# Performance work log

Measured on AMD Instinct MI355X. Metric: run time of the kernel, lower is better.

## Reference

```python
import jax, jax.numpy as jnp
import numpy as np

N_NODES, N_EDGES = 50000, 400000
F_IN, H, L, C = 8, 64, 3, 1
E_IN = 2 * H + 1 + 1  # feats_i, feats_j, edge_attr(1), rel_dist(1)


def setup_inputs() -> dict:
    key = jax.random.key(0)
    ks = jax.random.split(key, 16)
    s = 0.05
    return {
        "x": jax.random.normal(ks[0], (N_NODES, F_IN), jnp.float32),
        "pos": jax.random.normal(ks[1], (N_NODES, 3), jnp.float32),
        "edge_index": jax.random.randint(ks[2], (2, N_EDGES), 0, N_NODES),
        "edge_attr": jax.random.normal(ks[3], (N_EDGES, 1), jnp.float32),
        "embedW": jax.random.normal(ks[4], (F_IN, H), jnp.float32) * s,
        "embedb": jnp.zeros((H,), jnp.float32),
        "eW1": jax.random.normal(ks[5], (L, E_IN, 2 * E_IN), jnp.float32) * s,
        "eb1": jnp.zeros((L, 2 * E_IN), jnp.float32),
        "eW2": jax.random.normal(ks[6], (L, 2 * E_IN, H), jnp.float32) * s,
        "eb2": jnp.zeros((L, H), jnp.float32),
        "cW1": jax.random.normal(ks[7], (L, H, 4 * H), jnp.float32) * s,
        "cb1": jnp.zeros((L, 4 * H), jnp.float32),
        "cW2": jax.random.normal(ks[8], (L, 4 * H, 1), jnp.float32) * s,
        "cb2": jnp.zeros((L, 1), jnp.float32),
        "nW1": jax.random.normal(ks[9], (L, 2 * H, 2 * H), jnp.float32) * s,
        "nb1": jnp.zeros((L, 2 * H), jnp.float32),
        "nW2": jax.random.normal(ks[10], (L, 2 * H, H), jnp.float32) * s,
        "nb2": jnp.zeros((L, H), jnp.float32),
        "linW": jax.random.normal(ks[11], (H, C), jnp.float32) * s,
        "linb": jnp.zeros((C,), jnp.float32),
    }


def reference(x, pos, edge_index, edge_attr, embedW, embedb,
              eW1, eb1, eW2, eb2, cW1, cb1, cW2, cb2,
              nW1, nb1, nW2, nb2, linW, linb):
    silu = jax.nn.silu
    row, col = edge_index[0], edge_index[1]  # target i, source j
    feats = x @ embedW + embedb              # [N, H] initial node embedding
    coors = pos                              # [N, 3]
    for l in range(L):  # fixed small layer loop
        rel = coors[row] - coors[col]                            # [E, 3]
        dist = jnp.sum(rel * rel, axis=-1, keepdims=True)        # [E, 1]
        e_in = jnp.concatenate([feats[row], feats[col], edge_attr, dist], axis=-1)
        # edge_mlp: Linear -> SiLU -> Linear -> SiLU
        m = silu(silu(e_in @ eW1[l] + eb1[l]) @ eW2[l] + eb2[l])  # [E, H]
        # coors_mlp: Linear -> SiLU -> Linear -> scalar weight per edge
        cw = silu(m @ cW1[l] + cb1[l]) @ cW2[l] + cb2[l]          # [E, 1]
        coors = coors + jax.ops.segment_sum(cw * rel, row, num_segments=N_NODES)
        m_i = jax.ops.segment_sum(m, row, num_segments=N_NODES)  # [N, H]
        h = jnp.concatenate([feats, m_i], axis=-1)                # [N, 2H]
        # node_mlp: Linear -> SiLU -> Linear, residual on feats
        feats = feats + (silu(h @ nW1[l] + nb1[l]) @ nW2[l] + nb2[l])
    return feats @ linW + linb  # [N, C]
```

## Files before the change

kernel.cpp:

```cpp
#include <hip/hip_runtime.h>
#include <hip/hip_bf16.h>

#define NN 50000
#define NNP 50048
#define NE 400000
#define FH 64
#define NTILES (NE / 64)
#define CHUNK 782

typedef __attribute__((ext_vector_type(8))) short short8;
typedef __attribute__((ext_vector_type(8))) _Float16 half8;
typedef __attribute__((ext_vector_type(4))) float float4v;

__device__ __forceinline__ float silu_f(float x) {
    return x * __builtin_amdgcn_rcpf(1.0f + __expf(-x));
}
__device__ __forceinline__ short f2h(float f) {
    _Float16 h = (_Float16)f;
    return *(short*)&h;
}
__device__ __forceinline__ float h2f(short s) {
    _Float16 h = *(_Float16*)&s;
    return (float)h;
}

__device__ __forceinline__ void frag_body(const float* __restrict__ src,
                                          short* __restrict__ dst,
                                          int t, int K, int N, int KT, int dup,
                                          int perL, int srcL) {
    int l = t / perL, tt = t - l * perL;
    int j = tt & 7, lane = (tt >> 3) & 63, frag = tt >> 9;
    int nt = frag / KT, kt = frag - nt * KT;
    int k = kt * 32 + ((lane >> 4) << 3) + j;
    int n = nt * 16 + (lane & 15);
    if (k == dup) k = dup - 1;
    float v = (k < K && n < N) ? src[(size_t)l * srcL + k * N + n] : 0.f;
    dst[t] = f2h(v);
}

__global__ void prep_all(const float* __restrict__ eW1, const float* __restrict__ eW2,
                         const float* __restrict__ cW1, const float* __restrict__ nW1,
                         const float* __restrict__ nW2, const float* __restrict__ eb1,
                         short* W1f, short* W2f, short* cW1f, short* nW1f,
                         short* nW2f, float* b1p, int* __restrict__ deg) {
    int t = blockIdx.x * 256 + threadIdx.x;
    if (t < 130560) { frag_body(eW1, W1f, t, 131, 260, 5, 130, 43520, 33800); return; }
    t -= 130560;
    if (t < 55296) { frag_body(eW2, W2f, t, 260, 64, 9, -1, 18432, 16640); return; }
    t -= 55296;
    if (t < 49152) { frag_body(cW1, cW1f, t, 64, 256, 2, -1, 16384, 16384); return; }
    t -= 49152;
    if (t < 49152) { frag_body(nW1, nW1f, t, 128, 128, 4, -1, 16384, 16384); return; }
    t -= 49152;
    if (t < 24576) { frag_body(nW2, nW2f, t, 128, 64, 4, -1, 8192, 8192); return; }
    t -= 24576;
    if (t < 816) { int l = t / 272, c = t - l * 272; b1p[t] = (c < 260) ? eb1[l * 260 + c] : 0.f; return; }
    t -= 816;
    if (t < NN + 1) deg[t] = 0;
}

__global__ void embed_kernel(const float* __restrict__ x, const float* __restrict__ W,
                             const float* __restrict__ b, const float* __restrict__ pos,
                             float* __restrict__ feats, short* __restrict__ featsh,
                             float* __restrict__ cA) {
    int t = blockIdx.x * 256 + threadIdx.x;
    if (t >= NN * FH) return;
    int n = t >> 6, hcol = t & 63;
    float acc = b[hcol];
    #pragma unroll
    for (int k = 0; k < 8; k++) acc += x[n * 8 + k] * W[k * FH + hcol];
    feats[t] = acc;
    featsh[t] = f2h(acc);
    if (hcol < 3) cA[n * 3 + hcol] = pos[n * 3 + hcol];
}

__global__ void hist_kernel(const int* __restrict__ ei, int* __restrict__ deg) {
    int e = blockIdx.x * 256 + threadIdx.x;
    if (e >= NE) return;
    atomicAdd(&deg[ei[e]], 1);
}

__global__ void alloc_kernel(const int* __restrict__ deg, int* __restrict__ off,
                             int* __restrict__ cursor, int* __restrict__ gcount) {
    __shared__ int s[256];
    __shared__ int base;
    int t = threadIdx.x, n = blockIdx.x * 256 + t;
    int d = (n < NN) ? deg[n] : 0;
    s[t] = d;
    __syncthreads();
    for (int st = 1; st < 256; st <<= 1) {
        int v = (t >= st) ? s[t - st] : 0;
        __syncthreads();
        s[t] += v;
        __syncthreads();
    }
    if (t == 255) base = atomicAdd(gcount, s[255]);
    __syncthreads();
    if (n < NN) { int o = base + s[t] - d; off[n] = o; cursor[n] = o; }
}

__global__ void fill_kernel(const int* __restrict__ ei, const float* __restrict__ eattr,
                            int* __restrict__ cursor, int* __restrict__ erow,
                            int* __restrict__ ecol, float* __restrict__ eattrp) {
    int e = blockIdx.x * 256 + threadIdx.x;
    if (e >= NE) return;
    int r = ei[e];
    int p = atomicAdd(&cursor[r], 1);
    erow[p] = r;
    ecol[p] = ei[NE + e];
    eattrp[p] = eattr[e];
}

#define SE_STRIDE 168
#define H1_STRIDE 296
#define M_STRIDE  72

__global__ __launch_bounds__(256, 3) void edge_fused(
    const int* __restrict__ erow, const int* __restrict__ ecol,
    const float* __restrict__ eattrp,
    const short* __restrict__ featsh, const float* __restrict__ coors,
    const short* __restrict__ W1f, const float* __restrict__ b1p,
    const short* __restrict__ W2f, const float* __restrict__ b2,
    const short* __restrict__ cW1f, const float* __restrict__ cb1,
    const float* __restrict__ cW2, const float* __restrict__ cb2,
    short* __restrict__ m_edge, float* __restrict__ cwrel, int do_cw)
{
    __shared__ char smem[48896];
    short* sE   = (short*)smem;
    short* sH1  = (short*)smem;
    short* sM   = (short*)(smem + 37888);
    float* sRel = (float*)(smem + 47104);
    float* cwbuf = (float*)(smem + 47872);

    int b = blockIdx.x;
    int kb = (b & 7) * CHUNK + (b >> 3);
    if (kb >= NTILES) return;
    int k0 = kb * 64;

    int t = threadIdx.x;
    int lane = t & 63, wid = t >> 6, quad = lane >> 4, lc = lane & 15;

    {
        int el = t >> 2, sub = t & 3, k = k0 + el;
        int rI = erow[k], cI = ecol[k];
        const short8* fr = (const short8*)(featsh + (size_t)rI * FH);
        const short8* fc = (const short8*)(featsh + (size_t)cI * FH);
        short* er = sE + el * SE_STRIDE;
        *(short8*)(er + sub * 16) = fr[sub * 2];
        *(short8*)(er + sub * 16 + 8) = fr[sub * 2 + 1];
        *(short8*)(er + 64 + sub * 16) = fc[sub * 2];
        *(short8*)(er + 64 + sub * 16 + 8) = fc[sub * 2 + 1];
        #pragma unroll
        for (int i = 0; i < 10; i++) er[128 + sub * 10 + i] = 0;
        if (sub == 0) {
            float rx = coors[rI * 3 + 0] - coors[cI * 3 + 0];
            float ry = coors[rI * 3 + 1] - coors[cI * 3 + 1];
            float rz = coors[rI * 3 + 2] - coors[cI * 3 + 2];
            float dist = rx * rx + ry * ry + rz * rz;
            short dh = f2h(dist);
            er[128] = f2h(eattrp[k]);
            er[129] = dh;
            er[130] = f2h(dist - h2f(dh));
            sRel[el * 3 + 0] = rx; sRel[el * 3 + 1] = ry; sRel[el * 3 + 2] = rz;
        }
    }
    __syncthreads();

    half8 af[4][5];
    #pragma unroll
    for (int m = 0; m < 4; m++)
        #pragma unroll
        for (int kt = 0; kt < 5; kt++)
            af[m][kt] = *(const half8*)(sE + (m * 16 + lc) * SE_STRIDE + kt * 32 + quad * 8);
    __syncthreads();

    {
        *(long long*)(sH1 + (t >> 2) * H1_STRIDE + 272 + (t & 3) * 4) = 0LL;
        #pragma unroll
        for (int i = 0; i < 4; i++) {
            int nt = wid + i * 4;
            float bias = b1p[nt * 16 + lc];
            float4v acc[4];
            #pragma unroll
            for (int m = 0; m < 4; m++) acc[m] = (float4v){bias, bias, bias, bias};
            #pragma unroll
            for (int kt = 0; kt < 5; kt++) {
                half8 bh = ((const half8*)(W1f + (size_t)(nt * 5 + kt) * 512))[lane];
                #pragma unroll
                for (int m = 0; m < 4; m++)
                    acc[m] = __builtin_amdgcn_mfma_f32_16x16x32_f16(af[m][kt], bh, acc[m], 0, 0, 0);
            }
            #pragma unroll
            for (int m = 0; m < 4; m++)
                #pragma unroll
                for (int r = 0; r < 4; r++)
                    sH1[(m * 16 + quad * 4 + r) * H1_STRIDE + nt * 16 + lc] = f2h(silu_f(acc[m][r]));
        }
        if (wid == 0) {
            const int nt = 16;
            float bias = b1p[nt * 16 + lc];
            float4v acc[4];
            #pragma unroll
            for (int m = 0; m < 4; m++) acc[m] = (float4v){bias, bias, bias, bias};
            #pragma unroll
            for (int kt = 0; kt < 5; kt++) {
                half8 bh = ((const half8*)(W1f + (size_t)(nt * 5 + kt) * 512))[lane];
                #pragma unroll
                for (int m = 0; m < 4; m++)
                    acc[m] = __builtin_amdgcn_mfma_f32_16x16x32_f16(af[m][kt], bh, acc[m], 0, 0, 0);
            }
            #pragma unroll
            for (int m = 0; m < 4; m++)
                #pragma unroll
                for (int r = 0; r < 4; r++)
                    sH1[(m * 16 + quad * 4 + r) * H1_STRIDE + nt * 16 + lc] = f2h(silu_f(acc[m][r]));
        }
    }
    __syncthreads();

    {
        int nt = wid;
        float bias = b2[nt * 16 + lc];
        float4v acc[4];
        #pragma unroll
        for (int m = 0; m < 4; m++) acc[m] = (float4v){bias, bias, bias, bias};
        #pragma unroll
        for (int kt = 0; kt < 9; kt++) {
            half8 bh = ((const half8*)(W2f + (size_t)(nt * 9 + kt) * 512))[lane];
            #pragma unroll
            for (int m = 0; m < 4; m++) {
                half8 a = *(const half8*)(sH1 + (m * 16 + lc) * H1_STRIDE + kt * 32 + quad * 8);
                acc[m] = __builtin_amdgcn_mfma_f32_16x16x32_f16(a, bh, acc[m], 0, 0, 0);
            }
        }
        #pragma unroll
        for (int m = 0; m < 4; m++)
            #pragma unroll
            for (int r = 0; r < 4; r++)
                sM[(m * 16 + quad * 4 + r) * M_STRIDE + nt * 16 + lc] = f2h(silu_f(acc[m][r]));
    }
    __syncthreads();

    {
        int row = t >> 2, c0 = (t & 3) * 16;
        short8 v0 = *(const short8*)(sM + row * M_STRIDE + c0);
        short8 v1 = *(const short8*)(sM + row * M_STRIDE + c0 + 8);
        short* mg = m_edge + (size_t)(k0 + row) * FH + c0;
        *(short8*)(mg) = v0;
        *(short8*)(mg + 8) = v1;
    }
    if (do_cw) {
        half8 ag[4][2];
        #pragma unroll
        for (int m = 0; m < 4; m++)
            #pragma unroll
            for (int kt = 0; kt < 2; kt++)
                ag[m][kt] = *(const half8*)(sM + (m * 16 + lc) * M_STRIDE + kt * 32 + quad * 8);
        float cwpart[4][4];
        #pragma unroll
        for (int m = 0; m < 4; m++)
            #pragma unroll
            for (int r = 0; r < 4; r++) cwpart[m][r] = 0.f;
        #pragma unroll
        for (int i = 0; i < 4; i++) {
            int nt = wid + i * 4;
            float bias = cb1[nt * 16 + lc];
            float4v acc[4];
            #pragma unroll
            for (int m = 0; m < 4; m++) acc[m] = (float4v){bias, bias, bias, bias};
            #pragma unroll
            for (int kt = 0; kt < 2; kt++) {
                half8 bh = ((const half8*)(cW1f + (size_t)(nt * 2 + kt) * 512))[lane];
                #pragma unroll
                for (int m = 0; m < 4; m++)
                    acc[m] = __builtin_amdgcn_mfma_f32_16x16x32_f16(ag[m][kt], bh, acc[m], 0, 0, 0);
            }
            float wv = cW2[nt * 16 + lc];
            #pragma unroll
            for (int m = 0; m < 4; m++)
                #pragma unroll
                for (int r = 0; r < 4; r++)
                    cwpart[m][r] += silu_f(acc[m][r]) * wv;
        }
        #pragma unroll
        for (int m = 0; m < 4; m++)
            #pragma unroll
            for (int r = 0; r < 4; r++) {
                float p = cwpart[m][r];
                p += __shfl_xor(p, 1);
                p += __shfl_xor(p, 2);
                p += __shfl_xor(p, 4);
                p += __shfl_xor(p, 8);
                if (lc == 0) cwbuf[wid * 64 + m * 16 + quad * 4 + r] = p;
            }
        __syncthreads();

        if (t < 64) {
            float cw = cb2[0] + cwbuf[t] + cwbuf[64 + t] + cwbuf[128 + t] + cwbuf[192 + t];
            float* o = cwrel + (size_t)(k0 + t) * 3;
            o[0] = cw * sRel[t * 3 + 0];
            o[1] = cw * sRel[t * 3 + 1];
            o[2] = cw * sRel[t * 3 + 2];
        }
    }
}

#define HS 136
__global__ __launch_bounds__(256, 4) void agg_node(
    const int* __restrict__ off, const int* __restrict__ deg,
    const short* __restrict__ m_edge, const float* __restrict__ cwrel,
    const float* __restrict__ coors_in, float* __restrict__ coors_out,
    float* __restrict__ feats, short* __restrict__ featsh,
    const short* __restrict__ W1f, const float* __restrict__ b1,
    const short* __restrict__ W2f, const float* __restrict__ b2,
    const float* __restrict__ linW, const float* __restrict__ linb,
    float* __restrict__ out, int last)
{
    __shared__ short sh[64 * HS];
    __shared__ short sg[64 * HS];
    int t = threadIdx.x, lane = t & 63, wid = t >> 6, quad = lane >> 4, lc = lane & 15;
    int n0 = blockIdx.x * 64;

    {
        int row = t >> 2, sub = t & 3;
        const short8* fp = (const short8*)(featsh + (size_t)(n0 + row) * FH);
        *(short8*)(sh + row * HS + sub * 16) = fp[sub * 2];
        *(short8*)(sh + row * HS + sub * 16 + 8) = fp[sub * 2 + 1];
    }
    for (int nn = 0; nn < 16; nn++) {
        int row = wid * 16 + nn;
        int n = n0 + row;
        float sum = 0.f, cv = 0.f;
        if (n < NN) {
            int s = off[n], e = s + deg[n];
            float s0 = 0.f, s1 = 0.f, s2 = 0.f, s3 = 0.f;
            int k = s;
            for (; k + 3 < e; k += 4) {
                s0 += h2f(m_edge[(size_t)k * FH + lane]);
                s1 += h2f(m_edge[(size_t)(k + 1) * FH + lane]);
                s2 += h2f(m_edge[(size_t)(k + 2) * FH + lane]);
                s3 += h2f(m_edge[(size_t)(k + 3) * FH + lane]);
                if (!last && lane < 3)
                    cv += (cwrel[(size_t)k * 3 + lane] + cwrel[(size_t)(k + 1) * 3 + lane])
                        + (cwrel[(size_t)(k + 2) * 3 + lane] + cwrel[(size_t)(k + 3) * 3 + lane]);
            }
            for (; k < e; k++) {
                s0 += h2f(m_edge[(size_t)k * FH + lane]);
                if (!last && lane < 3) cv += cwrel[(size_t)k * 3 + lane];
            }
            sum = (s0 + s1) + (s2 + s3);
            if (!last && lane < 3) coors_out[n * 3 + lane] = coors_in[n * 3 + lane] + cv;
        }
        sh[row * HS + 64 + lane] = f2h(sum);
    }
    __syncthreads();

    half8 af[4][4];
    #pragma unroll
    for (int m = 0; m < 4; m++)
        #pragma unroll
        for (int kt = 0; kt < 4; kt++)
            af[m][kt] = *(const half8*)(sh + (m * 16 + lc) * HS + kt * 32 + quad * 8);
    #pragma unroll
    for (int i = 0; i < 2; i++) {
        int nt = wid + i * 4;
        float bias = b1[nt * 16 + lc];
        float4v acc[4];
        #pragma unroll
        for (int m = 0; m < 4; m++) acc[m] = (float4v){bias, bias, bias, bias};
        #pragma unroll
        for (int kt = 0; kt < 4; kt++) {
            half8 bh = ((const half8*)(W1f + (size_t)(nt * 4 + kt) * 512))[lane];
            #pragma unroll
            for (int m = 0; m < 4; m++)
                acc[m] = __builtin_amdgcn_mfma_f32_16x16x32_f16(af[m][kt], bh, acc[m], 0, 0, 0);
        }
        #pragma unroll
        for (int m = 0; m < 4; m++)
            #pragma unroll
            for (int r = 0; r < 4; r++)
                sg[(m * 16 + quad * 4 + r) * HS + nt * 16 + lc] = f2h(silu_f(acc[m][r]));
    }
    __syncthreads();

    {
        int nt = wid;
        float bias = b2[nt * 16 + lc];
        float4v acc[4];
        #pragma unroll
        for (int m = 0; m < 4; m++) acc[m] = (float4v){bias, bias, bias, bias};
        #pragma unroll
        for (int kt = 0; kt < 4; kt++) {
            half8 bh = ((const half8*)(W2f + (size_t)(nt * 4 + kt) * 512))[lane];
            #pragma unroll
            for (int m = 0; m < 4; m++) {
                half8 a = *(const half8*)(sg + (m * 16 + lc) * HS + kt * 32 + quad * 8);
                acc[m] = __builtin_amdgcn_mfma_f32_16x16x32_f16(a, bh, acc[m], 0, 0, 0);
            }
        }
        if (!last) {
            #pragma unroll
            for (int m = 0; m < 4; m++)
                #pragma unroll
                for (int r = 0; r < 4; r++) {
                    int row = m * 16 + quad * 4 + r;
                    size_t idx = (size_t)(n0 + row) * FH + nt * 16 + lc;
                    float nv = feats[idx] + acc[m][r];
                    feats[idx] = nv;
                    featsh[idx] = f2h(nv);
                }
        } else {
            float lw = linW[nt * 16 + lc];
            float v[4][4];
            #pragma unroll
            for (int m = 0; m < 4; m++)
                #pragma unroll
                for (int r = 0; r < 4; r++) {
                    int row = m * 16 + quad * 4 + r;
                    size_t idx = (size_t)(n0 + row) * FH + nt * 16 + lc;
                    v[m][r] = (feats[idx] + acc[m][r]) * lw;
                }
            __syncthreads();
            float* red = (float*)sg;
            #pragma unroll
            for (int m = 0; m < 4; m++)
                #pragma unroll
                for (int r = 0; r < 4; r++) {
                    float p = v[m][r];
                    p += __shfl_xor(p, 1);
                    p += __shfl_xor(p, 2);
                    p += __shfl_xor(p, 4);
                    p += __shfl_xor(p, 8);
                    if (lc == 0) red[(m * 16 + quad * 4 + r) * 4 + wid] = p;
                }
            __syncthreads();
            if (t < 64) {
                int n = n0 + t;
                if (n < NN)
                    out[n] = (red[t * 4 + 0] + red[t * 4 + 1])
                           + (red[t * 4 + 2] + red[t * 4 + 3]) + linb[0];
            }
        }
    }
}

extern "C" void kernel_launch(void* const* d_in, const int* in_sizes, int n_in,
                              void* d_out, int out_size, void* d_ws, size_t ws_size,
                              hipStream_t stream) {
    const float* x      = (const float*)d_in[0];
    const float* pos    = (const float*)d_in[1];
    const int*   ei     = (const int*)d_in[2];
    const float* eattr  = (const float*)d_in[3];
    const float* embedW = (const float*)d_in[4];
    const float* embedb = (const float*)d_in[5];
    const float* eW1    = (const float*)d_in[6];
    const float* eb1    = (const float*)d_in[7];
    const float* eW2    = (const float*)d_in[8];
    const float* eb2    = (const float*)d_in[9];
    const float* cW1    = (const float*)d_in[10];
    const float* cb1    = (const float*)d_in[11];
    const float* cW2    = (const float*)d_in[12];
    const float* cb2    = (const float*)d_in[13];
    const float* nW1    = (const float*)d_in[14];
    const float* nb1    = (const float*)d_in[15];
    const float* nW2    = (const float*)d_in[16];
    const float* nb2    = (const float*)d_in[17];
    const float* linW   = (const float*)d_in[18];
    const float* linb   = (const float*)d_in[19];
    float* out = (float*)d_out;

    char* wp = (char*)d_ws;
    auto alloc = [&](size_t bytes) { void* p = wp; wp += (bytes + 255) & ~(size_t)255; return p; };

    const int W1F_L  = 17 * 5 * 512;
    const int W2F_L  = 4 * 9 * 512;
    const int CW1F_L = 16 * 2 * 512;
    const int NW1F_L = 8 * 4 * 512;
    const int NW2F_L = 4 * 4 * 512;

    float* feats  = (float*)alloc((size_t)NNP * FH * 4);
    short* featsh = (short*)alloc((size_t)NNP * FH * 2);
    float* cA     = (float*)alloc((size_t)NN * 3 * 4);
    float* cB     = (float*)alloc((size_t)NN * 3 * 4);
    short* W1f    = (short*)alloc((size_t)3 * W1F_L * 2);
    short* W2f    = (short*)alloc((size_t)3 * W2F_L * 2);
    short* cW1f   = (short*)alloc((size_t)3 * CW1F_L * 2);
    short* nW1f   = (short*)alloc((size_t)3 * NW1F_L * 2);
    short* nW2f   = (short*)alloc((size_t)3 * NW2F_L * 2);
    float* b1p    = (float*)alloc((size_t)3 * 272 * 4);
    int*   deg    = (int*)alloc((size_t)(NN + 1) * 4);
    int*   off    = (int*)alloc((size_t)NN * 4);
    int*   cursor = (int*)alloc((size_t)NN * 4);
    int*   erow   = (int*)alloc((size_t)NE * 4);
    int*   ecol   = (int*)alloc((size_t)NE * 4);
    float* eattrp = (float*)alloc((size_t)NE * 4);
    short* m_edge = (short*)alloc((size_t)NE * FH * 2);
    float* cwrel  = (float*)alloc((size_t)NE * 3 * 4);
    int* gcount = deg + NN;

    prep_all<<<(359553 + 255) / 256, 256, 0, stream>>>(
        eW1, eW2, cW1, nW1, nW2, eb1,
        W1f, W2f, cW1f, nW1f, nW2f, b1p, deg);

    hist_kernel<<<(NE + 255) / 256, 256, 0, stream>>>(ei, deg);
    alloc_kernel<<<(NN + 255) / 256, 256, 0, stream>>>(deg, off, cursor, gcount);
    fill_kernel<<<(NE + 255) / 256, 256, 0, stream>>>(ei, eattr, cursor, erow, ecol, eattrp);

    embed_kernel<<<(NN * FH + 255) / 256, 256, 0, stream>>>(x, embedW, embedb, pos, feats, featsh, cA);

    float* ccur = cA;
    float* cnext = cB;
    for (int l = 0; l < 3; l++) {
        int last = (l == 2);
        edge_fused<<<8 * CHUNK, 256, 0, stream>>>(
            erow, ecol, eattrp, featsh, ccur,
            W1f + (size_t)l * W1F_L, b1p + l * 272,
            W2f + (size_t)l * W2F_L, eb2 + l * 64,
            cW1f + (size_t)l * CW1F_L, cb1 + l * 256,
            cW2 + l * 256, cb2 + l,
            m_edge, cwrel, last ? 0 : 1);
        agg_node<<<NNP / 64, 256, 0, stream>>>(
            off, deg, m_edge, cwrel, ccur, cnext, feats, featsh,
            nW1f + (size_t)l * NW1F_L, nb1 + l * 128,
            nW2f + (size_t)l * NW2F_L, nb2 + l * 64,
            linW, linb, out, last);
        float* tmp = ccur; ccur = cnext; cnext = tmp;
    }
}
```

Before: 582.2 us.

## Fuse segment-sum into edge kernel via run-length atomics on sorted rows

The edge kernel no longer writes per-edge messages and coordinate updates to global memory. Instead, each wave reduces consecutive edges that share a target row (edges are sorted by row) and issues float atomicAdds into a node-level m_i and coordinate-delta buffer. The node kernel then reads the pre-aggregated fp32 sums, converts them to half, zeroes the buffers for the next layer, and applies coordinate deltas in place. This removes the per-edge fp16 message round trip and the CSR gather, at the cost of atomic traffic, an fp32 node buffer, and non-deterministic summation order.

Result: no change. 591.9 us (+1.7%).

```diff
diff --git a/kernel.cpp b/kernel.cpp
--- a/kernel.cpp
+++ b/kernel.cpp
@@ -62,7 +62,7 @@
 __global__ void embed_kernel(const float* __restrict__ x, const float* __restrict__ W,
                              const float* __restrict__ b, const float* __restrict__ pos,
                              float* __restrict__ feats, short* __restrict__ featsh,
-                             float* __restrict__ cA) {
+                             float* __restrict__ coors) {
     int t = blockIdx.x * 256 + threadIdx.x;
     if (t >= NN * FH) return;
     int n = t >> 6, hcol = t & 63;
@@ -71,7 +71,7 @@
     for (int k = 0; k < 8; k++) acc += x[n * 8 + k] * W[k * FH + hcol];
     feats[t] = acc;
     featsh[t] = f2h(acc);
-    if (hcol < 3) cA[n * 3 + hcol] = pos[n * 3 + hcol];
+    if (hcol < 3) coors[n * 3 + hcol] = pos[n * 3 + hcol];
 }
 
 __global__ void hist_kernel(const int* __restrict__ ei, int* __restrict__ deg) {
@@ -123,7 +123,7 @@
     const short* __restrict__ W2f, const float* __restrict__ b2,
     const short* __restrict__ cW1f, const float* __restrict__ cb1,
     const float* __restrict__ cW2, const float* __restrict__ cb2,
-    short* __restrict__ m_edge, float* __restrict__ cwrel, int do_cw)
+    float* __restrict__ m_i, float* __restrict__ D, int do_cw)
 {
     __shared__ char smem[48896];
     short* sE   = (short*)smem;
@@ -241,14 +241,6 @@
     }
     __syncthreads();
 
-    {
-        int row = t >> 2, c0 = (t & 3) * 16;
-        short8 v0 = *(const short8*)(sM + row * M_STRIDE + c0);
-        short8 v1 = *(const short8*)(sM + row * M_STRIDE + c0 + 8);
-        short* mg = m_edge + (size_t)(k0 + row) * FH + c0;
-        *(short8*)(mg) = v0;
-        *(short8*)(mg + 8) = v1;
-    }
     if (do_cw) {
         half8 ag[4][2];
         #pragma unroll
@@ -294,22 +286,38 @@
                 if (lc == 0) cwbuf[wid * 64 + m * 16 + quad * 4 + r] = p;
             }
         __syncthreads();
-
-        if (t < 64) {
-            float cw = cb2[0] + cwbuf[t] + cwbuf[64 + t] + cwbuf[128 + t] + cwbuf[192 + t];
-            float* o = cwrel + (size_t)(k0 + t) * 3;
-            o[0] = cw * sRel[t * 3 + 0];
-            o[1] = cw * sRel[t * 3 + 1];
-            o[2] = cw * sRel[t * 3 + 2];
-        }
+        if (t < 64)
+            cwbuf[t] = cb2[0] + ((cwbuf[t] + cwbuf[64 + t]) + (cwbuf[128 + t] + cwbuf[192 + t]));
+        __syncthreads();
+    }
+
+    {
+        int cur = -1;
+        float s = 0.f, sc = 0.f;
+        #pragma unroll
+        for (int rr = 0; rr < 16; rr++) {
+            int r = wid * 16 + rr;
+            int rowid = erow[k0 + r];
+            float v = h2f(sM[r * M_STRIDE + lane]);
+            float c = 0.f;
+            if (do_cw && lane < 3) c = cwbuf[r] * sRel[r * 3 + lane];
+            if (rowid != cur) {
+                if (cur >= 0) {
+                    atomicAdd(&m_i[(size_t)cur * FH + lane], s);
+                    if (do_cw && lane < 3) atomicAdd(&D[cur * 3 + lane], sc);
+                }
+                cur = rowid; s = v; sc = c;
+            } else { s += v; sc += c; }
+        }
+        atomicAdd(&m_i[(size_t)cur * FH + lane], s);
+        if (do_cw && lane < 3) atomicAdd(&D[cur * 3 + lane], sc);
     }
 }
 
 #define HS 136
 __global__ __launch_bounds__(256, 4) void agg_node(
-    const int* __restrict__ off, const int* __restrict__ deg,
-    const short* __restrict__ m_edge, const float* __restrict__ cwrel,
-    const float* __restrict__ coors_in, float* __restrict__ coors_out,
+    float* __restrict__ m_i, float* __restrict__ D,
+    float* __restrict__ coors,
     float* __restrict__ feats, short* __restrict__ featsh,
     const short* __restrict__ W1f, const float* __restrict__ b1,
     const short* __restrict__ W2f, const float* __restrict__ b2,
@@ -323,35 +331,33 @@
 
     {
         int row = t >> 2, sub = t & 3;
-        const short8* fp = (const short8*)(featsh + (size_t)(n0 + row) * FH);
+        int n = n0 + row;
+        const short8* fp = (const short8*)(featsh + (size_t)n * FH);
         *(short8*)(sh + row * HS + sub * 16) = fp[sub * 2];
         *(short8*)(sh + row * HS + sub * 16 + 8) = fp[sub * 2 + 1];
-    }
-    for (int nn = 0; nn < 16; nn++) {
-        int row = wid * 16 + nn;
-        int n = n0 + row;
-        float sum = 0.f, cv = 0.f;
-        if (n < NN) {
-            int s = off[n], e = s + deg[n];
-            float s0 = 0.f, s1 = 0.f, s2 = 0.f, s3 = 0.f;
-            int k = s;
-            for (; k + 3 < e; k += 4) {
-                s0 += h2f(m_edge[(size_t)k * FH + lane]);
-                s1 += h2f(m_edge[(size_t)(k + 1) * FH + lane]);
-                s2 += h2f(m_edge[(size_t)(k + 2) * FH + lane]);
-                s3 += h2f(m_edge[(size_t)(k + 3) * FH + lane]);
-                if (!last && lane < 3)
-                    cv += (cwrel[(size_t)k * 3 + lane] + cwrel[(size_t)(k + 1) * 3 + lane])
-                        + (cwrel[(size_t)(k + 2) * 3 + lane] + cwrel[(size_t)(k + 3) * 3 + lane]);
-            }
-            for (; k < e; k++) {
-                s0 += h2f(m_edge[(size_t)k * FH + lane]);
-                if (!last && lane < 3) cv += cwrel[(size_t)k * 3 + lane];
-            }
-            sum = (s0 + s1) + (s2 + s3);
-            if (!last && lane < 3) coors_out[n * 3 + lane] = coors_in[n * 3 + lane] + cv;
-        }
-        sh[row * HS + 64 + lane] = f2h(sum);
+        float* mp = m_i + (size_t)n * FH + sub * 16;
+        float4 v0 = ((const float4*)mp)[0];
+        float4 v1 = ((const float4*)mp)[1];
+        float4 v2 = ((const float4*)mp)[2];
+        float4 v3 = ((const float4*)mp)[3];
+        short hb[16];
+        hb[0] = f2h(v0.x); hb[1] = f2h(v0.y); hb[2] = f2h(v0.z); hb[3] = f2h(v0.w);
+        hb[4] = f2h(v1.x); hb[5] = f2h(v1.y); hb[6] = f2h(v1.z); hb[7] = f2h(v1.w);
+        hb[8] = f2h(v2.x); hb[9] = f2h(v2.y); hb[10] = f2h(v2.z); hb[11] = f2h(v2.w);
+        hb[12] = f2h(v3.x); hb[13] = f2h(v3.y); hb[14] = f2h(v3.z); hb[15] = f2h(v3.w);
+        *(short8*)(sh + row * HS + 64 + sub * 16) = *(short8*)hb;
+        *(short8*)(sh + row * HS + 64 + sub * 16 + 8) = *(short8*)(hb + 8);
+        if (!last) {
+            float4 z = {0.f, 0.f, 0.f, 0.f};
+            ((float4*)mp)[0] = z; ((float4*)mp)[1] = z;
+            ((float4*)mp)[2] = z; ((float4*)mp)[3] = z;
+            if (sub == 0 && n < NN) {
+                coors[n * 3 + 0] += D[n * 3 + 0];
+                coors[n * 3 + 1] += D[n * 3 + 1];
+                coors[n * 3 + 2] += D[n * 3 + 2];
+                D[n * 3 + 0] = 0.f; D[n * 3 + 1] = 0.f; D[n * 3 + 2] = 0.f;
+            }
+        }
     }
     __syncthreads();
 
@@ -480,8 +486,9 @@
 
     float* feats  = (float*)alloc((size_t)NNP * FH * 4);
     short* featsh = (short*)alloc((size_t)NNP * FH * 2);
-    float* cA     = (float*)alloc((size_t)NN * 3 * 4);
-    float* cB     = (float*)alloc((size_t)NN * 3 * 4);
+    float* m_i    = (float*)alloc((size_t)NNP * FH * 4);
+    float* Dbuf   = (float*)alloc((size_t)NN * 3 * 4);
+    float* coorsb = (float*)alloc((size_t)NN * 3 * 4);
     short* W1f    = (short*)alloc((size_t)3 * W1F_L * 2);
     short* W2f    = (short*)alloc((size_t)3 * W2F_L * 2);
     short* cW1f   = (short*)alloc((size_t)3 * CW1F_L * 2);
@@ -494,8 +501,6 @@
     int*   erow   = (int*)alloc((size_t)NE * 4);
     int*   ecol   = (int*)alloc((size_t)NE * 4);
     float* eattrp = (float*)alloc((size_t)NE * 4);
-    short* m_edge = (short*)alloc((size_t)NE * FH * 2);
-    float* cwrel  = (float*)alloc((size_t)NE * 3 * 4);
     int* gcount = deg + NN;
 
     prep_all<<<(359553 + 255) / 256, 256, 0, stream>>>(
@@ -506,24 +511,24 @@
     alloc_kernel<<<(NN + 255) / 256, 256, 0, stream>>>(deg, off, cursor, gcount);
     fill_kernel<<<(NE + 255) / 256, 256, 0, stream>>>(ei, eattr, cursor, erow, ecol, eattrp);
 
-    embed_kernel<<<(NN * FH + 255) / 256, 256, 0, stream>>>(x, embedW, embedb, pos, feats, featsh, cA);
-
-    float* ccur = cA;
-    float* cnext = cB;
+    hipMemsetAsync(m_i, 0, (size_t)NNP * FH * 4, stream);
+    hipMemsetAsync(Dbuf, 0, (size_t)NN * 3 * 4, stream);
+
+    embed_kernel<<<(NN * FH + 255) / 256, 256, 0, stream>>>(x, embedW, embedb, pos, feats, featsh, coorsb);
+
     for (int l = 0; l < 3; l++) {
         int last = (l == 2);
         edge_fused<<<8 * CHUNK, 256, 0, stream>>>(
-            erow, ecol, eattrp, featsh, ccur,
+            erow, ecol, eattrp, featsh, coorsb,
             W1f + (size_t)l * W1F_L, b1p + l * 272,
             W2f + (size_t)l * W2F_L, eb2 + l * 64,
             cW1f + (size_t)l * CW1F_L, cb1 + l * 256,
             cW2 + l * 256, cb2 + l,
-            m_edge, cwrel, last ? 0 : 1);
+            m_i, Dbuf, last ? 0 : 1);
         agg_node<<<NNP / 64, 256, 0, stream>>>(
-            off, deg, m_edge, cwrel, ccur, cnext, feats, featsh,
+            m_i, Dbuf, coorsb, feats, featsh,
             nW1f + (size_t)l * NW1F_L, nb1 + l * 128,
             nW2f + (size_t)l * NW2F_L, nb2 + l * 64,
             linW, linb, out, last);
-        float* tmp = ccur; ccur = cnext; cnext = tmp;
-    }
-}
+    }
+}
```
